# Kernel optimization log

Hardware: AMD Instinct MI355X
Metric: run time of the kernel (lower is better)

Reference implementation:

```python
import jax, jax.numpy as jnp
import numpy as np

VOCAB, D, H = 50257, 128, 128  # embedding_dim=128, lstm_size=128, num_layers=1
B, T = 64, 2048


def setup_inputs() -> dict:
    key = jax.random.key(0)
    ks = jax.random.split(key, 6)
    s = 1.0 / np.sqrt(H)  # PyTorch LSTM init scale
    return {
        "tokens": jax.random.randint(ks[0], (B, T), 0, VOCAB, dtype=jnp.int32),
        "emb_table": jax.random.normal(ks[1], (VOCAB, D), dtype=jnp.float32),
        "W_ih": jax.random.uniform(ks[2], (4 * H, D), jnp.float32, -s, s),
        "W_hh": jax.random.uniform(ks[3], (4 * H, H), jnp.float32, -s, s),
        "b_ih": jax.random.uniform(ks[4], (4 * H,), jnp.float32, -s, s),
        "b_hh": jax.random.uniform(ks[5], (4 * H,), jnp.float32, -s, s),
    }


def reference(tokens, emb_table, W_ih, W_hh, b_ih, b_hh):
    # Embedding lookup for the whole sequence: [B, T, D] -> time-major [T, B, D]
    x = jnp.swapaxes(emb_table[tokens], 0, 1)
    b = b_ih + b_hh  # fuse the two bias adds
    xg = jnp.einsum('tbd,gd->tbg', x, W_ih) + b  # precompute input gates [T, B, 4H]

    def step(carry, xt):
        h, c = carry
        gates = xt + h @ W_hh.T  # [B, 4H], PyTorch gate order i,f,g,o
        i, f, g, o = jnp.split(gates, 4, axis=-1)
        c2 = jax.nn.sigmoid(f) * c + jax.nn.sigmoid(i) * jnp.tanh(g)
        h2 = jax.nn.sigmoid(o) * jnp.tanh(c2)
        return (h2, c2), None

    h0 = jnp.zeros((tokens.shape[0], H), dtype=x.dtype)
    (h, c), _ = jax.lax.scan(step, (h0, h0), xg)
    # Original returns (state_h, state_c) each [num_layers=1, batch, H]
    return h[None], c[None]
```

## Files before the change

kernel.cpp:

```cpp
#include <hip/hip_runtime.h>
#include <hip/hip_bf16.h>


namespace {

constexpr int T_LEN  = 2048;
constexpr int Bsz    = 64;
constexpr int Dd     = 128;
constexpr int Hh     = 128;
constexpr int Gg     = 512;
constexpr int XS     = 136;
constexpr int NCHUNK = 256;
constexpr int CONS   = 64;
constexpr int PROD   = 192;
constexpr unsigned int SENT = 0x5EC7C0DEu;

typedef __attribute__((ext_vector_type(8))) short   short8;
typedef __attribute__((ext_vector_type(4))) float   floatx4;
typedef __attribute__((ext_vector_type(4))) int     intx4;
typedef __attribute__((ext_vector_type(2))) unsigned int uintx2;

#define MFMA16(a, b, c) __builtin_amdgcn_mfma_f32_16x16x32_bf16((a), (b), (c), 0, 0, 0)

#if __has_builtin(__builtin_amdgcn_sdot4)
__device__ __forceinline__ int dot4i8(int a, int b, int c) {
    return __builtin_amdgcn_sdot4(a, b, c, false);
}
#else
__device__ __forceinline__ int dot4i8(int a, int b, int c) {
#pragma unroll
    for (int j = 0; j < 4; ++j)
        c += ((a << (24 - 8 * j)) >> 24) * ((b << (24 - 8 * j)) >> 24);
    return c;
}
#endif

__device__ __forceinline__ int xor1_i(int v) {
    return __builtin_amdgcn_mov_dpp(v, 0xB1, 0xF, 0xF, true);
}

__device__ __forceinline__ float sigmoidf_(float x) {
    return __builtin_amdgcn_rcpf(1.0f + __builtin_amdgcn_exp2f(x * -1.44269504f));
}
__device__ __forceinline__ float tanhf_(float x) {
    return __builtin_fmaf(-2.0f,
        __builtin_amdgcn_rcpf(1.0f + __builtin_amdgcn_exp2f(x * 2.88539008f)), 1.0f);
}
__device__ __forceinline__ unsigned short f2bf(float f) {
    __hip_bfloat16 h = __float2bfloat16(f);
    union { __hip_bfloat16 b; unsigned short u; } v; v.b = h; return v.u;
}
__device__ __forceinline__ float fi_(unsigned int u) {
    union { unsigned int u; float f; } v; v.u = u; return v.f;
}
__device__ __forceinline__ int f_as_i(float f) {
    union { float f; int i; } v; v.f = f; return v.i;
}
__device__ __forceinline__ float i_as_f(int i) {
    union { int i; float f; } v; v.i = i; return v.f;
}
__device__ __forceinline__ uintx2 f4bf(const float4 v) {
    union { unsigned short us[4]; uintx2 u2; } p;
    p.us[0] = f2bf(v.x); p.us[1] = f2bf(v.y); p.us[2] = f2bf(v.z); p.us[3] = f2bf(v.w);
    return p.u2;
}
__device__ __forceinline__ short8 ld8bf(const float* p) {
    const float4 a = *reinterpret_cast<const float4*>(p);
    const float4 b = *reinterpret_cast<const float4*>(p + 4);
    short8 s;
    s[0] = (short)f2bf(a.x); s[1] = (short)f2bf(a.y);
    s[2] = (short)f2bf(a.z); s[3] = (short)f2bf(a.w);
    s[4] = (short)f2bf(b.x); s[5] = (short)f2bf(b.y);
    s[6] = (short)f2bf(b.z); s[7] = (short)f2bf(b.w);
    return s;
}
__device__ __forceinline__ void lds_barrier() {
    asm volatile("s_waitcnt lgkmcnt(0)\n\ts_barrier" ::: "memory");
}
__device__ __forceinline__ void wait_chunk(const unsigned int* flags, int k) {
    while (__hip_atomic_load(&flags[k], __ATOMIC_RELAXED,
                             __HIP_MEMORY_SCOPE_AGENT) != SENT)
        __builtin_amdgcn_s_sleep(2);
    __builtin_amdgcn_fence(__ATOMIC_ACQUIRE, "agent");
}

__global__ __launch_bounds__(256) void lstm_fused_all(
    const int*   __restrict__ tokens,
    const float* __restrict__ emb,
    const float* __restrict__ Wih,
    const float* __restrict__ Whh,
    const float* __restrict__ bih,
    const float* __restrict__ bhh,
    unsigned short* __restrict__ xg,
    unsigned int*   __restrict__ flags,
    float*       __restrict__ out)
{
    __shared__ __align__(16) unsigned short albs[2][64 * XS];

    const int tid = threadIdx.x;

    if (blockIdx.x < CONS) {
        signed char (*hbuf)[128] =
            reinterpret_cast<signed char (*)[128]>(&albs[0][0]);

        const int wv = tid >> 6;
        const int l  = tid & 63;
        const int gh = l & 1;
        const int c  = wv * 32 + (l >> 1);
        const int b  = blockIdx.x;

        const float kf = gh ? 1.0f : 2.0f;
        const float kb = gh ? 0.0f : -1.0f;
        const int   sh = gh ? 0 : 16;

        int   wq[2][32];
        float dq[2];
#pragma unroll
        for (int q = 0; q < 2; ++q) {
            const int g = q * 2 + gh;
            const float* wr = Whh + (size_t)(g * 128 + c) * Hh;
            float am = 0.f;
#pragma unroll 8
            for (int k = 0; k < 128; k += 4) {
                const float4 v = *reinterpret_cast<const float4*>(wr + k);
                am = fmaxf(am, fmaxf(fmaxf(fabsf(v.x), fabsf(v.y)),
                                     fmaxf(fabsf(v.z), fabsf(v.w))));
            }
            const float swm = fmaxf(am, 1e-20f);
            dq[q] = swm * (1.0f / (127.0f * 127.0f));
            const float inv = 127.0f / swm;
#pragma unroll
            for (int d = 0; d < 32; ++d) {
                const float4 v = *reinterpret_cast<const float4*>(wr + d * 4);
                const int b0 = (int)__builtin_rintf(v.x * inv);
                const int b1 = (int)__builtin_rintf(v.y * inv);
                const int b2 = (int)__builtin_rintf(v.z * inv);
                const int b3 = (int)__builtin_rintf(v.w * inv);
                wq[q][d] = (b0 & 0xff) | ((b1 & 0xff) << 8) |
                           ((b2 & 0xff) << 16) | ((b3 & 0xff) << 24);
            }
        }

        intx4 hv[8];
#pragma unroll
        for (int j = 0; j < 8; ++j) hv[j] = (intx4){0, 0, 0, 0};

        const unsigned short* xptr = xg + (size_t)b * Gg + c * 4;
        const size_t xstride = (size_t)Bsz * Gg;

        wait_chunk(flags, 0);
        uintx2 xc[8], xcn[8];
#pragma unroll
        for (int u = 0; u < 8; ++u)
            xc[u] = *reinterpret_cast<const uintx2*>(xptr + (size_t)u * xstride);
        wait_chunk(flags, 1);

        float c_state = 0.0f;
        float h_last  = 0.0f;
        unsigned int fpre = SENT;

        for (int g = 0; g < NCHUNK; ++g) {
#pragma unroll
            for (int s = 0; s < 8; ++s) {
                if (s == 0) {
                    int tn = g + 1;
                    if (tn >= NCHUNK) tn = 0;
                    const size_t tb = (size_t)tn * 8;
#pragma unroll
                    for (int u = 0; u < 8; ++u)
                        xcn[u] = *reinterpret_cast<const uintx2*>(
                            xptr + (tb + u) * xstride);
                }
                if (s == 2) {
                    if (g + 2 < NCHUNK)
                        fpre = __hip_atomic_load(&flags[g + 2], __ATOMIC_RELAXED,
                                                 __HIP_MEMORY_SCOPE_AGENT);
                }
                if (s == 4) {
                    if (g + 2 < NCHUNK) {
                        if (fpre != SENT) wait_chunk(flags, g + 2);
                        else __builtin_amdgcn_fence(__ATOMIC_ACQUIRE, "agent");
                    }
                }

                int a0 = 0, a1 = 0, a2 = 0, a3 = 0;
                int b0 = 0, b1 = 0, b2 = 0, b3 = 0;
#pragma unroll
                for (int j = 0; j < 8; ++j) {
                    const intx4 h4 = hv[j];
                    a0 = dot4i8(wq[0][j * 4 + 0], h4[0], a0);
                    a1 = dot4i8(wq[0][j * 4 + 1], h4[1], a1);
                    a2 = dot4i8(wq[0][j * 4 + 2], h4[2], a2);
                    a3 = dot4i8(wq[0][j * 4 + 3], h4[3], a3);
                    b0 = dot4i8(wq[1][j * 4 + 0], h4[0], b0);
                    b1 = dot4i8(wq[1][j * 4 + 1], h4[1], b1);
                    b2 = dot4i8(wq[1][j * 4 + 2], h4[2], b2);
                    b3 = dot4i8(wq[1][j * 4 + 3], h4[3], b3);
                }
                const int m0 = (a0 + a1) + (a2 + a3);
                const int m1 = (b0 + b1) + (b2 + b3);

                const uintx2 xv = xc[s];
                const float x0 = fi_((xv.x << sh) & 0xffff0000u);
                const float x1 = fi_((xv.y << sh) & 0xffff0000u);
                const float g0 = (float)m0 * dq[0] + x0;
                const float g1 = (float)m1 * dq[1] + x1;

                const float r1 = sigmoidf_(g0);
                const float r2 = sigmoidf_(g1 * kf);
                const float v2 = __builtin_fmaf(r2, kf, kb);
                const float A  = r1 * v2;
                const float swv = i_as_f(xor1_i(f_as_i(gh ? r1 : A)));
                const float F   = gh ? r1 : swv;
                const float Ag  = gh ? swv : A;
                c_state = __builtin_fmaf(F, c_state, Ag);
                const float t2 = tanhf_(c_state);
                h_last = v2 * t2;

                const int nxt = (s & 1) ^ 1;
                if (gh == 1)
                    hbuf[nxt][c] =
                        (signed char)((int)__builtin_rintf(h_last * 127.0f));
                if (s == 7) {
#pragma unroll
                    for (int u = 0; u < 8; ++u) xc[u] = xcn[u];
                }
                lds_barrier();
#pragma unroll
                for (int j = 0; j < 8; ++j)
                    hv[j] = *reinterpret_cast<const intx4*>(
                        &hbuf[nxt][j * 16]);
            }
        }

        if (gh == 1) {
            out[b * Hh + c]            = h_last;
            out[Bsz * Hh + b * Hh + c] = c_state;
        }
    } else {
        const int pid  = blockIdx.x - CONS;
        const int wv   = tid >> 6;
        const int l    = tid & 63;
        const int quad = l >> 4;
        const int cl   = l & 15;
        const int srow = tid >> 2, sseg = tid & 3;

        float bias[2][4];
#pragma unroll
        for (int jj = 0; jj < 2; ++jj) {
            const int hhj = (wv * 2 + jj) * 16 + cl;
#pragma unroll
            for (int g = 0; g < 4; ++g)
                bias[jj][g] = bih[g * 128 + hhj] + bhh[g * 128 + hhj];
        }

        for (int chunk = pid; chunk < NCHUNK; chunk += PROD) {
            const int t0 = chunk * 8;

            {
                const int tok = tokens[srow * T_LEN + t0];
                const float* src = emb + (size_t)tok * Dd + sseg * 32;
#pragma unroll
                for (int p = 0; p < 4; ++p)
                    *reinterpret_cast<short8*>(
                        &albs[0][srow * XS + sseg * 32 + p * 8]) = ld8bf(src + p * 8);
            }
            __syncthreads();

            for (int tt = 0; tt < 8; ++tt) {
                const int cur = tt & 1, nxt = cur ^ 1;
                if (tt < 7) {
                    const int tok = tokens[srow * T_LEN + t0 + tt + 1];
                    const float* src = emb + (size_t)tok * Dd + sseg * 32;
#pragma unroll
                    for (int p = 0; p < 4; ++p)
                        *reinterpret_cast<short8*>(
                            &albs[nxt][srow * XS + sseg * 32 + p * 8]) =
                            ld8bf(src + p * 8);
                }

                short8 af[4][4];
#pragma unroll
                for (int m = 0; m < 4; ++m)
#pragma unroll
                    for (int k = 0; k < 4; ++k)
                        af[m][k] = *reinterpret_cast<const short8*>(
                            &albs[cur][(m * 16 + cl) * XS + k * 32 + quad * 8]);

                const int t = t0 + tt;
#pragma unroll
                for (int jj = 0; jj < 2; ++jj) {
                    const int hhj = (wv * 2 + jj) * 16 + cl;
                    floatx4 acc[4][4];
#pragma unroll
                    for (int g = 0; g < 4; ++g)
#pragma unroll
                        for (int m = 0; m < 4; ++m)
                            acc[g][m] = (floatx4){0.f, 0.f, 0.f, 0.f};
#pragma unroll
                    for (int g = 0; g < 4; ++g) {
                        const int n = g * 128 + hhj;
                        short8 bf[4];
#pragma unroll
                        for (int k = 0; k < 4; ++k)
                            bf[k] = ld8bf(Wih + (size_t)n * Dd + k * 32 + quad * 8);
#pragma unroll
                        for (int k = 0; k < 4; ++k)
#pragma unroll
                            for (int m = 0; m < 4; ++m)
                                acc[g][m] = MFMA16(af[m][k], bf[k], acc[g][m]);
                    }
#pragma unroll
                    for (int m = 0; m < 4; ++m) {
#pragma unroll
                        for (int r = 0; r < 4; ++r) {
                            const int brow = m * 16 + quad * 4 + r;
                            union { unsigned short us[4]; uintx2 u2; } p;
#pragma unroll
                            for (int g = 0; g < 4; ++g)
                                p.us[g] = f2bf(acc[g][m][r] + bias[jj][g]);
                            *reinterpret_cast<uintx2*>(
                                xg + ((size_t)t * Bsz + brow) * Gg + hhj * 4) =
                                p.u2;
                        }
                    }
                }
                __syncthreads();
            }

            if (tid == 0) {
                __builtin_amdgcn_fence(__ATOMIC_RELEASE, "agent");
                __hip_atomic_store(&flags[chunk], SENT, __ATOMIC_RELAXED,
                                   __HIP_MEMORY_SCOPE_AGENT);
            }
        }
    }
}

__global__ __launch_bounds__(512, 2) void lstm_fused_fb(
    const int*   __restrict__ tokens,
    const float* __restrict__ emb,
    const float* __restrict__ Wih,
    const float* __restrict__ Whh,
    const float* __restrict__ bih,
    const float* __restrict__ bhh,
    float*       __restrict__ out)
{
    __shared__ unsigned short xbuf[2][16 * XS];
    __shared__ unsigned short hbuf2[2][16 * XS];
    __shared__ float scratch[4 * Gg];

    const int tid  = threadIdx.x;
    const int w    = tid >> 6;
    const int l    = tid & 63;
    const int quad = l >> 4;
    const int cl   = l & 15;
    const int bbase = blockIdx.x * 4;
    const int rr = tid >> 7;
    const int hh = tid & 127;

    short8 wih[4][4], whh[4][4];
    float  bias[4];
#pragma unroll
    for (int q = 0; q < 4; ++q) {
        const int n = q * 128 + w * 16 + cl;
#pragma unroll
        for (int kk = 0; kk < 4; ++kk) {
            const int k0 = kk * 32 + quad * 8;
            wih[q][kk] = ld8bf(Wih + n * Dd + k0);
            whh[q][kk] = ld8bf(Whh + n * Hh + k0);
        }
        bias[q] = bih[n] + bhh[n];
    }

    for (int i = tid; i < 16 * XS; i += 512) {
        xbuf[0][i] = 0; xbuf[1][i] = 0; hbuf2[0][i] = 0; hbuf2[1][i] = 0;
    }

    const bool gact = (tid < 128);
    const int  gr = tid >> 5;
    const int  gp = tid & 31;
    float4 gdataf = {0.f, 0.f, 0.f, 0.f};
    if (gact) {
        const int tok = tokens[(bbase + gr) * T_LEN + 0];
        gdataf = *reinterpret_cast<const float4*>(emb + (size_t)tok * Dd + gp * 4);
    }
    __syncthreads();
    if (gact) *reinterpret_cast<uintx2*>(&xbuf[0][gr * XS + gp * 4]) = f4bf(gdataf);
    if (gact) {
        const int tok = tokens[(bbase + gr) * T_LEN + 1];
        gdataf = *reinterpret_cast<const float4*>(emb + (size_t)tok * Dd + gp * 4);
    }
    __syncthreads();

    const int afrag_el = cl * XS + quad * 8;

    floatx4 acc[4];
#pragma unroll
    for (int q = 0; q < 4; ++q) acc[q] = (floatx4){bias[q], bias[q], bias[q], bias[q]};
    {
        short8 xf[4];
#pragma unroll
        for (int kk = 0; kk < 4; ++kk)
            xf[kk] = *reinterpret_cast<const short8*>(&xbuf[0][afrag_el + kk * 32]);
#pragma unroll
        for (int kk = 0; kk < 4; ++kk)
#pragma unroll
            for (int q = 0; q < 4; ++q)
                acc[q] = MFMA16(xf[kk], wih[q][kk], acc[q]);
    }

    float c_state = 0.0f, h_last = 0.0f;

    for (int t = 0; t < T_LEN; ++t) {
        const int cur = t & 1, nxt = cur ^ 1;
        short8 hf[4];
#pragma unroll
        for (int kk = 0; kk < 4; ++kk)
            hf[kk] = *reinterpret_cast<const short8*>(&hbuf2[cur][afrag_el + kk * 32]);
        if (gact && (t + 1 < T_LEN))
            *reinterpret_cast<uintx2*>(&xbuf[nxt][gr * XS + gp * 4]) = f4bf(gdataf);
        if (gact && (t + 2 < T_LEN)) {
            const int tok = tokens[(bbase + gr) * T_LEN + (t + 2)];
            gdataf = *reinterpret_cast<const float4*>(emb + (size_t)tok * Dd + gp * 4);
        }
#pragma unroll
        for (int kk = 0; kk < 4; ++kk)
#pragma unroll
            for (int q = 0; q < 4; ++q)
                acc[q] = MFMA16(hf[kk], whh[q][kk], acc[q]);
        if (quad == 0) {
#pragma unroll
            for (int q = 0; q < 4; ++q) {
                const int n = q * 128 + w * 16 + cl;
#pragma unroll
                for (int r = 0; r < 4; ++r)
                    scratch[r * Gg + n] = acc[q][r];
            }
        }
        __syncthreads();
#pragma unroll
        for (int q = 0; q < 4; ++q) acc[q] = (floatx4){bias[q], bias[q], bias[q], bias[q]};
        if (t + 1 < T_LEN) {
            short8 xf[4];
#pragma unroll
            for (int kk = 0; kk < 4; ++kk)
                xf[kk] = *reinterpret_cast<const short8*>(&xbuf[nxt][afrag_el + kk * 32]);
#pragma unroll
            for (int kk = 0; kk < 4; ++kk)
#pragma unroll
                for (int q = 0; q < 4; ++q)
                    acc[q] = MFMA16(xf[kk], wih[q][kk], acc[q]);
        }
        {
            const float iv = scratch[rr * Gg + hh];
            const float fv = scratch[rr * Gg + 128 + hh];
            const float gv = scratch[rr * Gg + 256 + hh];
            const float ov = scratch[rr * Gg + 384 + hh];
            const float si = sigmoidf_(iv);
            const float sf = sigmoidf_(fv);
            const float so = sigmoidf_(ov);
            const float tg = tanhf_(gv);
            c_state = sf * c_state + si * tg;
            h_last  = so * tanhf_(c_state);
            hbuf2[nxt][rr * XS + hh] = f2bf(h_last);
        }
        __syncthreads();
    }

    const int ob = (bbase + rr) * Hh + hh;
    out[ob]            = h_last;
    out[Bsz * Hh + ob] = c_state;
}

}

extern "C" void kernel_launch(void* const* d_in, const int* in_sizes, int n_in,
                              void* d_out, int out_size, void* d_ws, size_t ws_size,
                              hipStream_t stream) {
    (void)in_sizes; (void)n_in; (void)out_size;
    const int*   tokens = (const int*)d_in[0];
    const float* emb    = (const float*)d_in[1];
    const float* Wih    = (const float*)d_in[2];
    const float* Whh    = (const float*)d_in[3];
    const float* bih    = (const float*)d_in[4];
    const float* bhh    = (const float*)d_in[5];

    const size_t xg_bytes = (size_t)T_LEN * Bsz * Gg * sizeof(unsigned short);
    const size_t need = xg_bytes + NCHUNK * sizeof(unsigned int);
    if (ws_size >= need) {
        unsigned short* xg    = (unsigned short*)d_ws;
        unsigned int*   flags = (unsigned int*)((char*)d_ws + xg_bytes);
        lstm_fused_all<<<CONS + PROD, 256, 0, stream>>>(
            tokens, emb, Wih, Whh, bih, bhh, xg, flags, (float*)d_out);
    } else {
        lstm_fused_fb<<<16, 512, 0, stream>>>(tokens, emb, Wih, Whh, bih, bhh,
                                              (float*)d_out);
    }
}
```

Before: 875.9 us.

## Replace per-step LDS barrier with sequence-counter spin polling in LSTM consumer

Replaces the per-timestep s_barrier in the recurrent consumer block with per-wave sequence counters in LDS. Each wave publishes its step number after writing its h slice. Readers spin, reading both the counters and the h buffer until all four waves reach the current step. The o-gate dot product and sigmoid are moved ahead of the i/f/g path, and h quantisation uses a magic-number FMA instead of rintf. The flag wait is moved from s==4 to s==6. With only double buffering and no barrier, the change relies on LDS ordering between the h write and the counter store, and it adds spin traffic.

```diff
diff --git a/kernel.cpp b/kernel.cpp
--- a/kernel.cpp
+++ b/kernel.cpp
@@ -73,9 +73,6 @@
     s[4] = (short)f2bf(b.x); s[5] = (short)f2bf(b.y);
     s[6] = (short)f2bf(b.z); s[7] = (short)f2bf(b.w);
     return s;
-}
-__device__ __forceinline__ void lds_barrier() {
-    asm volatile("s_waitcnt lgkmcnt(0)\n\ts_barrier" ::: "memory");
 }
 __device__ __forceinline__ void wait_chunk(const unsigned int* flags, int k) {
     while (__hip_atomic_load(&flags[k], __ATOMIC_RELAXED,
@@ -102,6 +99,8 @@
     if (blockIdx.x < CONS) {
         signed char (*hbuf)[128] =
             reinterpret_cast<signed char (*)[128]>(&albs[0][0]);
+        int* seqP = reinterpret_cast<int*>(
+            reinterpret_cast<char*>(&albs[0][0]) + 256);
 
         const int wv = tid >> 6;
         const int l  = tid & 63;
@@ -141,6 +140,9 @@
             }
         }
 
+        if (tid < 4) seqP[tid] = -1;
+        __syncthreads();
+
         intx4 hv[8];
 #pragma unroll
         for (int j = 0; j < 8; ++j) hv[j] = (intx4){0, 0, 0, 0};
@@ -162,6 +164,7 @@
         for (int g = 0; g < NCHUNK; ++g) {
 #pragma unroll
             for (int s = 0; s < 8; ++s) {
+                const int n = (g << 3) + s;
                 if (s == 0) {
                     int tn = g + 1;
                     if (tn >= NCHUNK) tn = 0;
@@ -176,15 +179,32 @@
                         fpre = __hip_atomic_load(&flags[g + 2], __ATOMIC_RELAXED,
                                                  __HIP_MEMORY_SCOPE_AGENT);
                 }
-                if (s == 4) {
+                if (s == 6) {
                     if (g + 2 < NCHUNK) {
                         if (fpre != SENT) wait_chunk(flags, g + 2);
                         else __builtin_amdgcn_fence(__ATOMIC_ACQUIRE, "agent");
                     }
                 }
 
+                int b0 = 0, b1 = 0, b2 = 0, b3 = 0;
+#pragma unroll
+                for (int j = 0; j < 8; ++j) {
+                    const intx4 h4 = hv[j];
+                    b0 = dot4i8(wq[1][j * 4 + 0], h4[0], b0);
+                    b1 = dot4i8(wq[1][j * 4 + 1], h4[1], b1);
+                    b2 = dot4i8(wq[1][j * 4 + 2], h4[2], b2);
+                    b3 = dot4i8(wq[1][j * 4 + 3], h4[3], b3);
+                }
+                const int m1 = (b0 + b1) + (b2 + b3);
+
+                const uintx2 xv = xc[s];
+                const float x1 = fi_((xv.y << sh) & 0xffff0000u);
+                const float g1 = (float)m1 * dq[1] + x1;
+                const float r2 = sigmoidf_(g1 * kf);
+                const float v2 = __builtin_fmaf(r2, kf, kb);
+                const float so127 = v2 * 127.0f;
+
                 int a0 = 0, a1 = 0, a2 = 0, a3 = 0;
-                int b0 = 0, b1 = 0, b2 = 0, b3 = 0;
 #pragma unroll
                 for (int j = 0; j < 8; ++j) {
                     const intx4 h4 = hv[j];
@@ -192,23 +212,12 @@
                     a1 = dot4i8(wq[0][j * 4 + 1], h4[1], a1);
                     a2 = dot4i8(wq[0][j * 4 + 2], h4[2], a2);
                     a3 = dot4i8(wq[0][j * 4 + 3], h4[3], a3);
-                    b0 = dot4i8(wq[1][j * 4 + 0], h4[0], b0);
-                    b1 = dot4i8(wq[1][j * 4 + 1], h4[1], b1);
-                    b2 = dot4i8(wq[1][j * 4 + 2], h4[2], b2);
-                    b3 = dot4i8(wq[1][j * 4 + 3], h4[3], b3);
                 }
                 const int m0 = (a0 + a1) + (a2 + a3);
-                const int m1 = (b0 + b1) + (b2 + b3);
-
-                const uintx2 xv = xc[s];
+
                 const float x0 = fi_((xv.x << sh) & 0xffff0000u);
-                const float x1 = fi_((xv.y << sh) & 0xffff0000u);
                 const float g0 = (float)m0 * dq[0] + x0;
-                const float g1 = (float)m1 * dq[1] + x1;
-
                 const float r1 = sigmoidf_(g0);
-                const float r2 = sigmoidf_(g1 * kf);
-                const float v2 = __builtin_fmaf(r2, kf, kb);
                 const float A  = r1 * v2;
                 const float swv = i_as_f(xor1_i(f_as_i(gh ? r1 : A)));
                 const float F   = gh ? r1 : swv;
@@ -218,18 +227,41 @@
                 h_last = v2 * t2;
 
                 const int nxt = (s & 1) ^ 1;
-                if (gh == 1)
-                    hbuf[nxt][c] =
-                        (signed char)((int)__builtin_rintf(h_last * 127.0f));
+                if (gh == 1) {
+                    const int q =
+                        f_as_i(__builtin_fmaf(so127, t2, 12582912.0f));
+                    hbuf[nxt][c] = (signed char)(q & 0xff);
+                }
+                if (l == 1)
+                    __hip_atomic_store(&seqP[wv], n, __ATOMIC_RELEASE,
+                                       __HIP_MEMORY_SCOPE_WORKGROUP);
                 if (s == 7) {
 #pragma unroll
                     for (int u = 0; u < 8; ++u) xc[u] = xcn[u];
                 }
-                lds_barrier();
-#pragma unroll
-                for (int j = 0; j < 8; ++j)
-                    hv[j] = *reinterpret_cast<const intx4*>(
-                        &hbuf[nxt][j * 16]);
+
+                {
+                    const unsigned hoff = (unsigned)(nxt << 7);
+                    intx4 s4;
+                    do {
+                        asm volatile(
+                            "ds_read_b128 %0, %9 offset:256\n\t"
+                            "ds_read_b128 %1, %10\n\t"
+                            "ds_read_b128 %2, %10 offset:16\n\t"
+                            "ds_read_b128 %3, %10 offset:32\n\t"
+                            "ds_read_b128 %4, %10 offset:48\n\t"
+                            "ds_read_b128 %5, %10 offset:64\n\t"
+                            "ds_read_b128 %6, %10 offset:80\n\t"
+                            "ds_read_b128 %7, %10 offset:96\n\t"
+                            "ds_read_b128 %8, %10 offset:112\n\t"
+                            "s_waitcnt lgkmcnt(0)"
+                            : "=&v"(s4), "=&v"(hv[0]), "=&v"(hv[1]),
+                              "=&v"(hv[2]), "=&v"(hv[3]), "=&v"(hv[4]),
+                              "=&v"(hv[5]), "=&v"(hv[6]), "=&v"(hv[7])
+                            : "v"(0u), "v"(hoff)
+                            : "memory");
+                    } while (s4[0] < n || s4[1] < n || s4[2] < n || s4[3] < n);
+                }
             }
         }
 
```

After: 1.002 ms. 14.4% more time.
